# Performance work log

Hardware: AMD Instinct MI355X
Metric: run time of the kernel (lower is better)

Reference implementation:

```python
import jax, jax.numpy as jnp
import numpy as np

B, N, D, H, DH = 4, 2048, 512, 8, 64  # batch, seqlen, hidden, heads, dim-per-head
EPS = 1e-5


def _layer_norm(x, g, b):
    m = jnp.mean(x, axis=-1, keepdims=True)
    v = jnp.var(x, axis=-1, keepdims=True)
    return (x - m) * jax.lax.rsqrt(v + EPS) * g + b


def setup_inputs() -> dict:
    key = jax.random.key(0)
    k0, k1, k2 = jax.random.split(key, 3)
    T = B * N
    return {
        "x": jax.random.normal(k0, (T, D), jnp.float32),
        "ln1_g": jnp.ones((D,), jnp.float32),
        "ln1_b": jnp.zeros((D,), jnp.float32),
        "w_uvqk": jax.random.normal(k1, (D, H * 4 * DH), jnp.float32) * 0.02,
        "ln2_g": jnp.ones((H * DH,), jnp.float32),
        "ln2_b": jnp.zeros((H * DH,), jnp.float32),
        "w_proj": jax.random.normal(k2, (H * DH, D), jnp.float32) * 0.02,
        "scaling_seqlen": N,
    }


def reference(x, ln1_g, ln1_b, w_uvqk, ln2_g, ln2_b, w_proj, scaling_seqlen):
    T = x.shape[0]
    # input layernorm -> fused uvqk projection -> SiLU
    normed_x = _layer_norm(x, ln1_g, ln1_b)
    silu_uvqk = jax.nn.silu(normed_x @ w_uvqk)          # [T, H*4*DH]
    silu_uvqk = silu_uvqk.reshape(T, H, 4 * DH)
    user, value, query, key = jnp.split(silu_uvqk, [DH, 2 * DH, 3 * DH], axis=-1)

    # jagged -> [B, N, H, DH] (equal-length sequences, offsets = i*N)
    q = query.reshape(B, N, H, DH)
    k = key.reshape(B, N, H, DH)
    v = value.reshape(B, N, H, DH)

    # HSTU attention: silu-gated (no softmax), causal, scaled by 1/scaling_seqlen
    scores = jnp.einsum('bnhd,bmhd->bhnm', q, k)        # [B, H, N, N]
    p = jax.nn.silu(scores) / jnp.float32(scaling_seqlen)
    causal = jnp.tril(jnp.ones((N, N), bool))
    p = jnp.where(causal, p, 0.0)
    attn = jnp.einsum('bhnm,bmhd->bnhd', p, v).reshape(T, H * DH)

    # output norm, user gate, projection, residual (dropout p=0.0 -> identity)
    normed_attn = _layer_norm(attn, ln2_g, ln2_b)
    user_flat = user.reshape(T, H * DH)
    out = (normed_attn * user_flat) @ w_proj + x
    return out
```

## Files before the change

kernel.cpp:

```cpp
#include <hip/hip_runtime.h>
#include <hip/hip_bf16.h>

typedef __bf16 bf16;
typedef __attribute__((ext_vector_type(8))) __bf16 bf16x8;
typedef __attribute__((ext_vector_type(4))) float f32x4;
typedef __attribute__((ext_vector_type(16))) float f32x16;

#define BB   4
#define NN   2048
#define DD   512
#define HH   8
#define DHH  64
#define TT   (BB*NN)
#define NUU  (HH*4*DHH)

#define AS1 __attribute__((address_space(1)))
#define AS3 __attribute__((address_space(3)))
__device__ __forceinline__ void gload16(const void* g, void* l){
  __builtin_amdgcn_global_load_lds((const AS1 void*)g, (AS3 void*)l, 16, 0, 0);
}

__device__ __forceinline__ float silu_fast(float x){
  return x * __builtin_amdgcn_rcpf(1.0f + __expf(-x));
}

__device__ __forceinline__ unsigned pk2(float a, float b){
  return (unsigned)__builtin_bit_cast(unsigned short, (bf16)a)
       | ((unsigned)__builtin_bit_cast(unsigned short, (bf16)b) << 16);
}

__device__ __forceinline__ void plswap(unsigned &a, unsigned &b){
  asm volatile("v_permlane32_swap_b32 %0, %1" : "+v"(a), "+v"(b));
}

__constant__ unsigned ATBL[24] = {
  7u|(0u<<4)|(16u<<10), 15u|(0u<<4)|(16u<<10), 14u|(0u<<4)|(15u<<10), 14u|(15u<<4)|(15u<<10),
  6u|(0u<<4)|(14u<<10), 13u|(0u<<4)|(14u<<10), 12u|(0u<<4)|(13u<<10), 11u|(0u<<4)|(12u<<10),
  15u|(16u<<4)|(16u<<10), 13u|(14u<<4)|(14u<<10), 12u|(13u<<4)|(13u<<10), 10u|(0u<<4)|(11u<<10),
  10u|(11u<<4)|(11u<<10), 9u|(0u<<4)|(10u<<10), 5u|(0u<<4)|(12u<<10), 11u|(12u<<4)|(12u<<10),
  0u|(0u<<4)|(2u<<10), 1u|(0u<<4)|(4u<<10), 2u|(0u<<4)|(6u<<10), 3u|(0u<<4)|(8u<<10),
  8u|(0u<<4)|(9u<<10), 9u|(10u<<4)|(10u<<10), 8u|(9u<<4)|(9u<<10), 4u|(0u<<4)|(10u<<10)
};

__global__ void k_transpose2(const float* __restrict__ w1, bf16* __restrict__ o1,
                             const float* __restrict__ w2, bf16* __restrict__ o2){
  __shared__ float tile[32][33];
  int tx = threadIdx.x, ty = threadIdx.y;
  int bx = blockIdx.x;
  const float* in; bf16* out; int R, C, c0;
  if (bx < 64){ in = w1; out = o1; R = 512; C = 2048; c0 = bx*32; }
  else        { in = w2; out = o2; R = 512; C = 512;  c0 = (bx-64)*32; }
  int r0 = blockIdx.y*32;
  #pragma unroll
  for (int i=0;i<4;i++) tile[ty+i*8][tx] = in[(size_t)(r0+ty+i*8)*C + c0+tx];
  __syncthreads();
  #pragma unroll
  for (int i=0;i<4;i++) out[(size_t)(c0+ty+i*8)*R + r0+tx] = (bf16)tile[tx][ty+i*8];
}

__global__ void k_ln_cast(const float* __restrict__ x, const float* __restrict__ g,
                          const float* __restrict__ bta, bf16* __restrict__ out){
  int lane = threadIdx.x & 63;
  int row  = blockIdx.x*4 + (threadIdx.x>>6);
  const float* xr = x + (size_t)row*512 + lane*8;
  float4 v0 = *(const float4*)xr;
  float4 v1 = *(const float4*)(xr+4);
  float vv[8] = {v0.x,v0.y,v0.z,v0.w,v1.x,v1.y,v1.z,v1.w};
  float s = 0.f, ss = 0.f;
  #pragma unroll
  for (int j=0;j<8;j++){ s += vv[j]; ss += vv[j]*vv[j]; }
  #pragma unroll
  for (int d=32; d; d>>=1){ s += __shfl_xor(s,d); ss += __shfl_xor(ss,d); }
  float m  = s * (1.f/512.f);
  float vr = ss * (1.f/512.f) - m*m;
  float rs = rsqrtf(vr + 1e-5f);
  const float* gp = g + lane*8;
  const float* bp = bta + lane*8;
  bf16x8 o;
  #pragma unroll
  for (int j=0;j<8;j++) o[j] = (bf16)((vv[j]-m)*rs*gp[j] + bp[j]);
  *(bf16x8*)(out + (size_t)row*512 + lane*8) = o;
}

__global__ void k_ln_gate(const float* __restrict__ attn0, const float* __restrict__ attn1,
                          const float* __restrict__ g, const float* __restrict__ bta,
                          const bf16* __restrict__ uvqk, bf16* __restrict__ out){
  int lane = threadIdx.x & 63;
  int row  = blockIdx.x*4 + (threadIdx.x>>6);
  const float* xr = attn0 + (size_t)row*512 + lane*8;
  float4 v0 = *(const float4*)xr;
  float4 v1 = *(const float4*)(xr+4);
  float vv[8] = {v0.x,v0.y,v0.z,v0.w,v1.x,v1.y,v1.z,v1.w};
  if (((row & (NN-1)) >> 7) >= 8){
    const float* x2 = attn1 + (size_t)row*512 + lane*8;
    float4 w0 = *(const float4*)x2;
    float4 w1 = *(const float4*)(x2+4);
    vv[0]+=w0.x; vv[1]+=w0.y; vv[2]+=w0.z; vv[3]+=w0.w;
    vv[4]+=w1.x; vv[5]+=w1.y; vv[6]+=w1.z; vv[7]+=w1.w;
  }
  float s = 0.f, ss = 0.f;
  #pragma unroll
  for (int j=0;j<8;j++){ s += vv[j]; ss += vv[j]*vv[j]; }
  #pragma unroll
  for (int d=32; d; d>>=1){ s += __shfl_xor(s,d); ss += __shfl_xor(ss,d); }
  float m  = s * (1.f/512.f);
  float vr = ss * (1.f/512.f) - m*m;
  float rs = rsqrtf(vr + 1e-5f);
  const float* gp = g + lane*8;
  const float* bp = bta + lane*8;
  const bf16* up = uvqk + (size_t)row*NUU + (lane>>3)*256 + ((lane*8)&63);
  bf16x8 uu = *(const bf16x8*)up;
  bf16x8 o;
  #pragma unroll
  for (int j=0;j<8;j++)
    o[j] = (bf16)(((vv[j]-m)*rs*gp[j] + bp[j]) * (float)uu[j]);
  *(bf16x8*)(out + (size_t)row*512 + lane*8) = o;
}

template<int EPI>
__global__ __launch_bounds__(256) void k_gemm(const bf16* __restrict__ A,
                                              const bf16* __restrict__ BT,
                                              int Nd, const float* __restrict__ resid,
                                              void* __restrict__ Cout,
                                              bf16* __restrict__ vtout){
  __shared__ __align__(16) char smem[32768];
  char* As = smem;
  char* Bs = smem + 16384;
  const int K = 512;
  int t = threadIdx.x, lane = t & 63, wid = t >> 6;
  int wr = wid >> 1, wc = wid & 1;
  int lin = blockIdx.x;
  int wk  = (lin & 7)*((int)gridDim.x >> 3) + (lin >> 3);
  int nx  = Nd >> 7;
  int m0 = (wk / nx) * 128, n0 = (wk % nx) * 128;
  int blk = (lane & 7) ^ (lane >> 3);
  const bf16* gA = A  + (size_t)(m0 + wid*32 + (lane>>3))*K + blk*8;
  const bf16* gB = BT + (size_t)(n0 + wid*32 + (lane>>3))*K + blk*8;
  f32x4 acc[4][4] = {};
  for (int k0 = 0; k0 < K; k0 += 64){
    __syncthreads();
    #pragma unroll
    for (int c = 0; c < 4; ++c){
      gload16(gA + (size_t)c*8*K, As + wid*4096 + c*1024);
      gload16(gB + (size_t)c*8*K, Bs + wid*4096 + c*1024);
    }
    gA += 64; gB += 64;
    __syncthreads();
    #pragma unroll
    for (int kk = 0; kk < 64; kk += 32){
      int c0 = kk + (lane >> 4) * 8;
      bf16x8 a[4], b[4];
      #pragma unroll
      for (int i = 0; i < 4; i++){
        int ra = wr*64 + i*16 + (lane & 15);
        a[i] = *(const bf16x8*)(As + (((ra*64 + c0)*2) ^ ((ra & 7) << 4)));
        int rb = wc*64 + i*16 + (lane & 15);
        b[i] = *(const bf16x8*)(Bs + (((rb*64 + c0)*2) ^ ((rb & 7) << 4)));
      }
      #pragma unroll
      for (int i = 0; i < 4; i++)
        #pragma unroll
        for (int jj = 0; jj < 4; jj++)
          acc[i][jj] = __builtin_amdgcn_mfma_f32_16x16x32_bf16(a[i], b[jj], acc[i][jj], 0, 0, 0);
    }
  }
  bool isv = (EPI == 0) && ((n0 & 255) == 0) && (wc == 1);
  #pragma unroll
  for (int i = 0; i < 4; i++){
    #pragma unroll
    for (int jj = 0; jj < 4; jj++){
      int col = n0 + wc*64 + jj*16 + (lane & 15);
      if (EPI == 0){
        union { unsigned long long u; ushort s[4]; } pw;
        #pragma unroll
        for (int r = 0; r < 4; r++){
          int rowg = m0 + wr*64 + i*16 + (lane >> 4)*4 + r;
          float sv = silu_fast(acc[i][jj][r]);
          ((bf16*)Cout)[(size_t)rowg*Nd + col] = (bf16)sv;
          pw.s[r] = __builtin_bit_cast(ushort, (bf16)sv);
        }
        if (isv){
          int dh    = jj*16 + (lane & 15);
          int rowg0 = m0 + wr*64 + i*16 + (lane >> 4)*4;
          int bb = rowg0 >> 11, nn = rowg0 & (NN-1);
          int hh = n0 >> 8;
          *(unsigned long long*)(vtout + ((size_t)((bb*HH + hh)*64 + dh)*NN + nn)) = pw.u;
        }
      } else {
        #pragma unroll
        for (int r = 0; r < 4; r++){
          int rowg = m0 + wr*64 + i*16 + (lane >> 4)*4 + r;
          ((float*)Cout)[(size_t)rowg*Nd + col] = acc[i][jj][r] + resid[(size_t)rowg*Nd + col];
        }
      }
    }
  }
}

__global__ __launch_bounds__(256, 4) void k_attn(const bf16* __restrict__ uv,
                                                 const bf16* __restrict__ vt,
                                                 float* __restrict__ attn0,
                                                 float* __restrict__ attn1,
                                                 const int* __restrict__ scal){
  __shared__ __align__(16) char smem[32768];
  int t = threadIdx.x, lane = t & 63, w = t >> 6;
  int hi5 = lane >> 5;
  int l31 = lane & 31;
  int lin = blockIdx.x;
  int pos = lin & 255;
  int grp = pos & 31;
  int rank = (lin >> 8)*8 + (pos >> 5);
  unsigned e = ATBL[rank];
  int qt = e & 15;
  int j0 = (int)((e >> 4) & 63);
  int j1 = j0 + (int)(e >> 10) - 1;
  float* ob = j0 ? attn1 : attn0;
  int b = grp >> 3, h = grp & 7;
  int tok0 = b*NN + qt*128;
  float sinv = 1.0f / (float)(scal[0]);

  int blk  = (lane & 7) ^ (lane >> 3);
  int rsub = lane >> 3;

  bf16x8 qfrag[4];
  {
    const bf16* gq = uv + (size_t)(tok0 + w*32 + l31)*NUU + h*256 + 128 + hi5*8;
    #pragma unroll
    for (int ks = 0; ks < 4; ++ks)
      qfrag[ks] = *(const bf16x8*)(gq + ks*16);
  }
  const bf16* gk = uv + (size_t)(b*NN + j0*64 + w*16 + rsub)*NUU + h*256 + 192 + blk*8;
  const bf16* gv = vt + (size_t)((b*HH + h)*64 + w*16 + rsub)*NN + j0*64 + blk*8;
  gload16(gk,                  smem + w*2048);
  gload16(gk + (size_t)8*NUU,  smem + w*2048 + 1024);
  gload16(gv,                  smem + 8192 + w*2048);
  gload16(gv + (size_t)8*NN,   smem + 8192 + w*2048 + 1024);
  gk += (size_t)64*NUU; gv += 64;

  f32x16 oacc[2] = {};
  int qmin  = qt*128 + w*32;
  int qglob = qmin + l31;
  int cur = 0;
  for (int j = j0; j <= j1; ++j){
    if (j < j1){
      gload16(gk,                 smem + (cur^1)*16384 + w*2048);
      gload16(gk + (size_t)8*NUU, smem + (cur^1)*16384 + w*2048 + 1024);
      gload16(gv,                 smem + (cur^1)*16384 + 8192 + w*2048);
      gload16(gv + (size_t)8*NN,  smem + (cur^1)*16384 + 8192 + w*2048 + 1024);
      gk += (size_t)64*NUU; gv += 64;
      asm volatile("s_waitcnt vmcnt(4)" ::: "memory");
    } else {
      asm volatile("s_waitcnt vmcnt(0)" ::: "memory");
    }
    __builtin_amdgcn_s_barrier();
    const char* Ks = smem + cur*16384;
    const char* Vs = Ks + 8192;
    #pragma unroll
    for (int sub = 0; sub < 2; ++sub){
      int kvbase = j*64 + sub*32;
      if (kvbase < qmin + 32){
        f32x16 sacc = {};
        int rk = sub*32 + l31;
        #pragma unroll
        for (int ks = 0; ks < 4; ++ks){
          int c0 = ks*16 + hi5*8;
          bf16x8 ak = *(const bf16x8*)(Ks + (((rk*64 + c0)*2) ^ ((rk & 7) << 4)));
          sacc = __builtin_amdgcn_mfma_f32_32x32x16_bf16(ak, qfrag[ks], sacc, 0, 0, 0);
        }
        union { unsigned u[8]; bf16x8 v[2]; } P;
        if (kvbase + 31 <= qmin){
          #pragma unroll
          for (int m = 0; m < 4; ++m){
            P.u[2*m]   = pk2(silu_fast(sacc[4*m+0]), silu_fast(sacc[4*m+1]));
            P.u[2*m+1] = pk2(silu_fast(sacc[4*m+2]), silu_fast(sacc[4*m+3]));
          }
        } else {
          #pragma unroll
          for (int m = 0; m < 4; ++m){
            float pr[4];
            #pragma unroll
            for (int r = 0; r < 4; ++r){
              int kvg = kvbase + 8*m + 4*hi5 + r;
              pr[r] = (kvg <= qglob) ? silu_fast(sacc[4*m+r]) : 0.0f;
            }
            P.u[2*m]   = pk2(pr[0], pr[1]);
            P.u[2*m+1] = pk2(pr[2], pr[3]);
          }
        }
        plswap(P.u[0], P.u[2]); plswap(P.u[1], P.u[3]);
        plswap(P.u[4], P.u[6]); plswap(P.u[5], P.u[7]);
        #pragma unroll
        for (int kh = 0; kh < 2; ++kh){
          int c0 = sub*32 + kh*16 + hi5*8;
          #pragma unroll
          for (int dsb = 0; dsb < 2; ++dsb){
            int rv = dsb*32 + l31;
            bf16x8 vb = *(const bf16x8*)(Vs + (((rv*64 + c0)*2) ^ ((rv & 7) << 4)));
            oacc[dsb] = __builtin_amdgcn_mfma_f32_32x32x16_bf16(P.v[kh], vb, oacc[dsb], 0, 0, 0);
          }
        }
      }
    }
    asm volatile("" ::: "memory");
    __builtin_amdgcn_s_barrier();
    cur ^= 1;
  }
  #pragma unroll
  for (int dsb = 0; dsb < 2; ++dsb){
    #pragma unroll
    for (int r = 0; r < 16; ++r){
      int qrow = (r & 3) + 4*hi5 + 8*(r >> 2);
      ob[(size_t)(tok0 + w*32 + qrow)*DD + h*64 + dsb*32 + l31] = oacc[dsb][r] * sinv;
    }
  }
}

extern "C" void kernel_launch(void* const* d_in, const int* in_sizes, int n_in,
                              void* d_out, int out_size, void* d_ws, size_t ws_size,
                              hipStream_t stream){
  (void)in_sizes; (void)n_in; (void)out_size; (void)ws_size;
  const float* x      = (const float*)d_in[0];
  const float* ln1_g  = (const float*)d_in[1];
  const float* ln1_b  = (const float*)d_in[2];
  const float* w_uvqk = (const float*)d_in[3];
  const float* ln2_g  = (const float*)d_in[4];
  const float* ln2_b  = (const float*)d_in[5];
  const float* w_proj = (const float*)d_in[6];
  const int*   scal   = (const int*)d_in[7];
  float* out = (float*)d_out;

  char* ws = (char*)d_ws;
  bf16*  wT1  = (bf16*)(ws);
  bf16*  wT2  = (bf16*)(ws + (2u<<20));
  bf16*  xn   = (bf16*)(ws + (2u<<20) + (512u<<10));
  bf16*  uvq  = (bf16*)(ws + (10u<<20) + (512u<<10));
  float* attn = (float*)(ws + (42u<<20) + (512u<<10));
  bf16*  vtb  = (bf16*)(ws + (58u<<20) + (512u<<10));
  float* attn1= (float*)(ws + (66u<<20) + (512u<<10));

  k_transpose2<<<dim3(80,16), dim3(32,8), 0, stream>>>(w_uvqk, wT1, w_proj, wT2);
  k_ln_cast<<<TT/4, 256, 0, stream>>>(x, ln1_g, ln1_b, xn);
  k_gemm<0><<<dim3(1024), dim3(256), 0, stream>>>(xn, wT1, 2048, nullptr, (void*)uvq, vtb);
  k_attn<<<dim3(768), dim3(256), 0, stream>>>(uvq, vtb, attn, attn1, scal);
  k_ln_gate<<<TT/4, 256, 0, stream>>>(attn, attn1, ln2_g, ln2_b, uvq, xn);
  k_gemm<1><<<dim3(256), dim3(256), 0, stream>>>(xn, wT2, 512, x, (void*)out, nullptr);
}
```

Measured before the change: 98.61 us.

## Split causal attention KV range into fixed 8-tile chunks across more blocks

Replaces the hand-tuned table of 24 work items with a uniform split: each query tile is broken into chunks of at most 8 KV tiles, giving 40 work items per batch-head and 1280 blocks. Partial results go to four separate fp32 buffers that the LN/gate kernel adds together. The change also raises the occupancy hint to 5 blocks per CU and wraps the MFMA sections in s_setprio. The aim is better load balance and occupancy, at the cost of more partial-sum traffic and extra reads in the LN kernel.

```diff
diff --git a/kernel.cpp b/kernel.cpp
--- a/kernel.cpp
+++ b/kernel.cpp
@@ -32,15 +32,6 @@
 __device__ __forceinline__ void plswap(unsigned &a, unsigned &b){
   asm volatile("v_permlane32_swap_b32 %0, %1" : "+v"(a), "+v"(b));
 }
-
-__constant__ unsigned ATBL[24] = {
-  7u|(0u<<4)|(16u<<10), 15u|(0u<<4)|(16u<<10), 14u|(0u<<4)|(15u<<10), 14u|(15u<<4)|(15u<<10),
-  6u|(0u<<4)|(14u<<10), 13u|(0u<<4)|(14u<<10), 12u|(0u<<4)|(13u<<10), 11u|(0u<<4)|(12u<<10),
-  15u|(16u<<4)|(16u<<10), 13u|(14u<<4)|(14u<<10), 12u|(13u<<4)|(13u<<10), 10u|(0u<<4)|(11u<<10),
-  10u|(11u<<4)|(11u<<10), 9u|(0u<<4)|(10u<<10), 5u|(0u<<4)|(12u<<10), 11u|(12u<<4)|(12u<<10),
-  0u|(0u<<4)|(2u<<10), 1u|(0u<<4)|(4u<<10), 2u|(0u<<4)|(6u<<10), 3u|(0u<<4)|(8u<<10),
-  8u|(0u<<4)|(9u<<10), 9u|(10u<<4)|(10u<<10), 8u|(9u<<4)|(9u<<10), 4u|(0u<<4)|(10u<<10)
-};
 
 __global__ void k_transpose2(const float* __restrict__ w1, bf16* __restrict__ o1,
                              const float* __restrict__ w2, bf16* __restrict__ o2){
@@ -83,18 +74,32 @@
 }
 
 __global__ void k_ln_gate(const float* __restrict__ attn0, const float* __restrict__ attn1,
+                          const float* __restrict__ attn2, const float* __restrict__ attn3,
                           const float* __restrict__ g, const float* __restrict__ bta,
                           const bf16* __restrict__ uvqk, bf16* __restrict__ out){
   int lane = threadIdx.x & 63;
   int row  = blockIdx.x*4 + (threadIdx.x>>6);
-  const float* xr = attn0 + (size_t)row*512 + lane*8;
+  size_t off = (size_t)row*512 + lane*8;
+  const float* xr = attn0 + off;
   float4 v0 = *(const float4*)xr;
   float4 v1 = *(const float4*)(xr+4);
   float vv[8] = {v0.x,v0.y,v0.z,v0.w,v1.x,v1.y,v1.z,v1.w};
-  if (((row & (NN-1)) >> 7) >= 8){
-    const float* x2 = attn1 + (size_t)row*512 + lane*8;
-    float4 w0 = *(const float4*)x2;
-    float4 w1 = *(const float4*)(x2+4);
+  int qtile = (row & (NN-1)) >> 7;
+  if (qtile >= 4){
+    const float* x2 = attn1 + off;
+    float4 w0 = *(const float4*)x2, w1 = *(const float4*)(x2+4);
+    vv[0]+=w0.x; vv[1]+=w0.y; vv[2]+=w0.z; vv[3]+=w0.w;
+    vv[4]+=w1.x; vv[5]+=w1.y; vv[6]+=w1.z; vv[7]+=w1.w;
+  }
+  if (qtile >= 8){
+    const float* x2 = attn2 + off;
+    float4 w0 = *(const float4*)x2, w1 = *(const float4*)(x2+4);
+    vv[0]+=w0.x; vv[1]+=w0.y; vv[2]+=w0.z; vv[3]+=w0.w;
+    vv[4]+=w1.x; vv[5]+=w1.y; vv[6]+=w1.z; vv[7]+=w1.w;
+  }
+  if (qtile >= 12){
+    const float* x2 = attn3 + off;
+    float4 w0 = *(const float4*)x2, w1 = *(const float4*)(x2+4);
     vv[0]+=w0.x; vv[1]+=w0.y; vv[2]+=w0.z; vv[3]+=w0.w;
     vv[4]+=w1.x; vv[5]+=w1.y; vv[6]+=w1.z; vv[7]+=w1.w;
   }
@@ -114,7 +119,7 @@
   #pragma unroll
   for (int j=0;j<8;j++)
     o[j] = (bf16)(((vv[j]-m)*rs*gp[j] + bp[j]) * (float)uu[j]);
-  *(bf16x8*)(out + (size_t)row*512 + lane*8) = o;
+  *(bf16x8*)(out + off) = o;
 }
 
 template<int EPI>
@@ -197,25 +202,31 @@
   }
 }
 
-__global__ __launch_bounds__(256, 4) void k_attn(const bf16* __restrict__ uv,
+__global__ __launch_bounds__(256, 5) void k_attn(const bf16* __restrict__ uv,
                                                  const bf16* __restrict__ vt,
                                                  float* __restrict__ attn0,
                                                  float* __restrict__ attn1,
+                                                 float* __restrict__ attn2,
+                                                 float* __restrict__ attn3,
                                                  const int* __restrict__ scal){
   __shared__ __align__(16) char smem[32768];
   int t = threadIdx.x, lane = t & 63, w = t >> 6;
   int hi5 = lane >> 5;
   int l31 = lane & 31;
-  int lin = blockIdx.x;
-  int pos = lin & 255;
-  int grp = pos & 31;
-  int rank = (lin >> 8)*8 + (pos >> 5);
-  unsigned e = ATBL[rank];
-  int qt = e & 15;
-  int j0 = (int)((e >> 4) & 63);
-  int j1 = j0 + (int)(e >> 10) - 1;
-  float* ob = j0 ? attn1 : attn0;
+  int lin  = blockIdx.x;
+  int work = (lin & 7)*160 + (lin >> 3);
+  int grp  = work / 40;
+  int d    = 39 - (work % 40);
   int b = grp >> 3, h = grp & 7;
+  int qt, ch;
+  if (d < 4)       { qt = d;              ch = 0; }
+  else if (d < 12) { qt = 4  + (d-4)/2;   ch = (d-4)&1; }
+  else if (d < 24) { qt = 8  + (d-12)/3;  ch = (d-12)%3; }
+  else             { qt = 12 + (d-24)/4;  ch = (d-24)&3; }
+  int j0 = ch*8;
+  int jmax = 2*qt + 1;
+  int j1 = (jmax < j0+7) ? jmax : j0+7;
+  float* ob = (ch==0) ? attn0 : (ch==1) ? attn1 : (ch==2) ? attn2 : attn3;
   int tok0 = b*NN + qt*128;
   float sinv = 1.0f / (float)(scal[0]);
 
@@ -261,12 +272,14 @@
       if (kvbase < qmin + 32){
         f32x16 sacc = {};
         int rk = sub*32 + l31;
+        __builtin_amdgcn_s_setprio(1);
         #pragma unroll
         for (int ks = 0; ks < 4; ++ks){
           int c0 = ks*16 + hi5*8;
           bf16x8 ak = *(const bf16x8*)(Ks + (((rk*64 + c0)*2) ^ ((rk & 7) << 4)));
           sacc = __builtin_amdgcn_mfma_f32_32x32x16_bf16(ak, qfrag[ks], sacc, 0, 0, 0);
         }
+        __builtin_amdgcn_s_setprio(0);
         union { unsigned u[8]; bf16x8 v[2]; } P;
         if (kvbase + 31 <= qmin){
           #pragma unroll
@@ -289,6 +302,7 @@
         }
         plswap(P.u[0], P.u[2]); plswap(P.u[1], P.u[3]);
         plswap(P.u[4], P.u[6]); plswap(P.u[5], P.u[7]);
+        __builtin_amdgcn_s_setprio(1);
         #pragma unroll
         for (int kh = 0; kh < 2; ++kh){
           int c0 = sub*32 + kh*16 + hi5*8;
@@ -299,6 +313,7 @@
             oacc[dsb] = __builtin_amdgcn_mfma_f32_32x32x16_bf16(P.v[kh], vb, oacc[dsb], 0, 0, 0);
           }
         }
+        __builtin_amdgcn_s_setprio(0);
       }
     }
     asm volatile("" ::: "memory");
@@ -334,14 +349,16 @@
   bf16*  wT2  = (bf16*)(ws + (2u<<20));
   bf16*  xn   = (bf16*)(ws + (2u<<20) + (512u<<10));
   bf16*  uvq  = (bf16*)(ws + (10u<<20) + (512u<<10));
-  float* attn = (float*)(ws + (42u<<20) + (512u<<10));
+  float* attn0= (float*)(ws + (42u<<20) + (512u<<10));
   bf16*  vtb  = (bf16*)(ws + (58u<<20) + (512u<<10));
   float* attn1= (float*)(ws + (66u<<20) + (512u<<10));
+  float* attn2= (float*)(ws + (82u<<20) + (512u<<10));
+  float* attn3= (float*)(ws + (98u<<20) + (512u<<10));
 
   k_transpose2<<<dim3(80,16), dim3(32,8), 0, stream>>>(w_uvqk, wT1, w_proj, wT2);
   k_ln_cast<<<TT/4, 256, 0, stream>>>(x, ln1_g, ln1_b, xn);
   k_gemm<0><<<dim3(1024), dim3(256), 0, stream>>>(xn, wT1, 2048, nullptr, (void*)uvq, vtb);
-  k_attn<<<dim3(768), dim3(256), 0, stream>>>(uvq, vtb, attn, attn1, scal);
-  k_ln_gate<<<TT/4, 256, 0, stream>>>(attn, attn1, ln2_g, ln2_b, uvq, xn);
+  k_attn<<<dim3(1280), dim3(256), 0, stream>>>(uvq, vtb, attn0, attn1, attn2, attn3, scal);
+  k_ln_gate<<<TT/4, 256, 0, stream>>>(attn0, attn1, attn2, attn3, ln2_g, ln2_b, uvq, xn);
   k_gemm<1><<<dim3(256), dim3(256), 0, stream>>>(xn, wT2, 512, x, (void*)out, nullptr);
 }
```

After: 104.9 us. 6.3% more time.
